# Optimization experiments

Hardware: AMD Instinct MI355X
Metric: run time of the kernel (lower is better)

## Reference

```python
import jax, jax.numpy as jnp
import numpy as np

B, L, HID, H = 4, 1024, 1024, 16
D = HID // H  # 64

def setup_inputs() -> dict:
    key = jax.random.key(0)
    ks = jax.random.split(key, 9)
    s = 0.02
    return {
        'query_states': jax.random.normal(ks[0], (B, L, HID), jnp.float32),
        'key_states':   jax.random.normal(ks[1], (B, L, HID), jnp.float32),
        'value_states': jax.random.normal(ks[2], (B, L, HID), jnp.float32),
        'Wq': jax.random.normal(ks[3], (HID, HID), jnp.float32) * s,
        'bq': jnp.zeros((HID,), jnp.float32),
        'Wk': jax.random.normal(ks[4], (HID, HID), jnp.float32) * s,
        'bk': jnp.zeros((HID,), jnp.float32),
        'Wv': jax.random.normal(ks[5], (HID, HID), jnp.float32) * s,
        'bv': jnp.zeros((HID,), jnp.float32),
        'Wo': jax.random.normal(ks[6], (HID, HID), jnp.float32) * s,
        'bo': jnp.zeros((HID,), jnp.float32),
        'rel_pos_enc': jax.random.normal(ks[7], (2 * L - 1, D), jnp.float32),
    }

def _split_heads(x):
    # [B,L,HID] -> [B,H,L,D]
    return x.reshape(B, L, H, D).transpose(0, 2, 1, 3)

def reference(query_states, key_states, value_states, Wq, bq, Wk, bk, Wv, bv, Wo, bo, rel_pos_enc):
    q = _split_heads(query_states @ Wq + bq)  # [B,H,L,D]
    k = _split_heads(key_states @ Wk + bk)
    v = _split_heads(value_states @ Wv + bv)
    scores = jnp.einsum('bhld,bhrd->bhlr', q, k)
    # relative position bias
    pos = jnp.arange(L)
    distance = pos[:, None] - pos[None, :] + L - 1          # [L,L] in [0, 2L-2]
    pos_emb = rel_pos_enc[distance]                          # [L,L,D]
    scores = scores + jnp.einsum('bhld,lrd->bhlr', q, pos_emb)
    scores = scores / jnp.sqrt(jnp.asarray(D, scores.dtype))
    probs = jax.nn.softmax(scores, axis=-1)                  # dropout p=0 (eval)
    ctx = jnp.einsum('bhlr,bhrd->bhld', probs, v)
    ctx = ctx.transpose(0, 2, 1, 3).reshape(B, L, HID)
    out = ctx @ Wo + bo
    return (out, probs)
```

## Files before the change

### kernel.cpp

```cpp
#include <hip/hip_runtime.h>

typedef __bf16 bf16_t;
typedef bf16_t bf16x8 __attribute__((ext_vector_type(8)));
typedef bf16_t bf16x4 __attribute__((ext_vector_type(4)));
typedef float f32x16 __attribute__((ext_vector_type(16)));
typedef float f32x4v __attribute__((ext_vector_type(4)));
typedef unsigned int u32;

#define DEVI __device__ __forceinline__

DEVI f32x16 zero16() {
  f32x16 z;
#pragma unroll
  for (int i = 0; i < 16; ++i) z[i] = 0.0f;
  return z;
}

DEVI void gload16(const bf16_t* g, const unsigned short* l) {
  __builtin_amdgcn_global_load_lds(
      (const __attribute__((address_space(1))) u32*)g,
      (__attribute__((address_space(3))) u32*)l, 16, 0, 0);
}

union U16B { bf16x8 v; uint4 u; unsigned short s[8]; };
union U4B  { bf16_t h[4]; uint2 u; };

__global__ __launch_bounds__(256) void prep_kernel(
    const float* __restrict__ W0, const float* __restrict__ W1,
    const float* __restrict__ W2, const float* __restrict__ W3,
    bf16_t* __restrict__ T0, bf16_t* __restrict__ T1,
    bf16_t* __restrict__ T2, bf16_t* __restrict__ T3,
    const float* __restrict__ xq, const float* __restrict__ xk,
    const float* __restrict__ xv, const float* __restrict__ relE,
    bf16_t* __restrict__ xqb, bf16_t* __restrict__ xkb,
    bf16_t* __restrict__ xvb, bf16_t* __restrict__ Eb) {
  __shared__ float T[64][65];
  const int bid = blockIdx.x;
  const int tid = threadIdx.x;
  if (bid < 1024) {
    const int sel = bid >> 8;
    const float* W = sel == 0 ? W0 : sel == 1 ? W1 : sel == 2 ? W2 : W3;
    bf16_t* Wt = sel == 0 ? T0 : sel == 1 ? T1 : sel == 2 ? T2 : T3;
    const int bx = bid & 255;
    const int tx = bx & 15, ty = bx >> 4;
    const int k0 = ty * 64, n0 = tx * 64;
    {
      const int r = tid >> 4, c4 = (tid & 15) * 4;
#pragma unroll
      for (int rr = 0; rr < 64; rr += 16) {
        float4 v = *reinterpret_cast<const float4*>(&W[(size_t)(k0 + r + rr) * 1024 + n0 + c4]);
        T[r + rr][c4 + 0] = v.x; T[r + rr][c4 + 1] = v.y;
        T[r + rr][c4 + 2] = v.z; T[r + rr][c4 + 3] = v.w;
      }
    }
    __syncthreads();
    {
      const int r = tid >> 3, c8 = (tid & 7) * 8;
#pragma unroll
      for (int rr = 0; rr < 64; rr += 32) {
        U16B p;
#pragma unroll
        for (int i = 0; i < 8; ++i) p.v[i] = (bf16_t)T[c8 + i][r + rr];
        *reinterpret_cast<uint4*>(&Wt[(size_t)(n0 + r + rr) * 1024 + k0 + c8]) = p.u;
      }
    }
  } else {
    for (int u = (bid - 1024) * 256 + tid; u < 3178496; u += 2048 * 256) {
      if (u < 3145728) {
        const int which = u >> 20;
        const float* src = which == 0 ? xq : which == 1 ? xk : xv;
        bf16_t* dst = which == 0 ? xqb : which == 1 ? xkb : xvb;
        const size_t off = (size_t)(u & 1048575) * 4;
        float4 v = *reinterpret_cast<const float4*>(&src[off]);
        U4B p;
        p.h[0] = (bf16_t)v.x; p.h[1] = (bf16_t)v.y; p.h[2] = (bf16_t)v.z; p.h[3] = (bf16_t)v.w;
        *reinterpret_cast<uint2*>(&dst[off]) = p.u;
      } else {
        const int q = u - 3145728;
        U4B p;
        if (q < 32752) {
          float4 v = *reinterpret_cast<const float4*>(&relE[(size_t)q * 4]);
          p.h[0] = (bf16_t)v.x; p.h[1] = (bf16_t)v.y; p.h[2] = (bf16_t)v.z; p.h[3] = (bf16_t)v.w;
        } else {
          p.h[0] = p.h[1] = p.h[2] = p.h[3] = (bf16_t)0.0f;
        }
        *reinterpret_cast<uint2*>(&Eb[(size_t)q * 4]) = p.u;
      }
    }
  }
}

#define ROWMAP(reg) (((reg) & 3) + 8 * ((reg) >> 2) + 4 * hi)

__global__ __launch_bounds__(512, 2) void gemm_qkv_kernel(
    const bf16_t* __restrict__ A0, const bf16_t* __restrict__ A1,
    const bf16_t* __restrict__ A2, const bf16_t* __restrict__ W0,
    const bf16_t* __restrict__ W1, const bf16_t* __restrict__ W2,
    const float* __restrict__ b0, const float* __restrict__ b1,
    const float* __restrict__ b2, bf16_t* __restrict__ O0,
    bf16_t* __restrict__ O1, bf16_t* __restrict__ O2) {
  __shared__ __align__(16) unsigned short As[2][256][64];
  __shared__ __align__(16) unsigned short Bs[2][256][64];
  const int f = blockIdx.x;
  const int fp = (f & 7) * 24 + (f >> 3);
  const int op = fp >> 6;
  const int r = fp & 63;
  const bf16_t* Ap = op == 0 ? A0 : op == 1 ? A1 : A2;
  const bf16_t* Wt = op == 0 ? W0 : op == 1 ? W1 : W2;
  const float* bias = op == 0 ? b0 : op == 1 ? b1 : b2;
  bf16_t* Out = op == 0 ? O0 : op == 1 ? O1 : O2;
  const int m0 = (r >> 2) * 256, n0 = (r & 3) * 256;
  const int tid = threadIdx.x;
  const int lane = tid & 63, wave = tid >> 6;
  const int hi = lane >> 5, ln = lane & 31;
  const int wr = wave >> 2, wc = wave & 3;
  const int srow = lane >> 3, scol = lane & 7;

  f32x16 acc[4][2];
#pragma unroll
  for (int rt = 0; rt < 4; ++rt) { acc[rt][0] = zero16(); acc[rt][1] = zero16(); }

#define STAGE(kt, buf)                                                              \
  {                                                                                 \
    _Pragma("unroll")                                                               \
    for (int j = 0; j < 4; ++j) {                                                   \
      const int rowbase = wave * 32 + j * 8;                                        \
      const int row = rowbase + srow;                                               \
      const int gc = scol ^ (row & 7);                                              \
      gload16(&Ap[(size_t)(m0 + row) * 1024 + (kt) * 64 + gc * 8],                  \
              &As[buf][rowbase][0]);                                                \
      gload16(&Wt[(size_t)(n0 + row) * 1024 + (kt) * 64 + gc * 8],                  \
              &Bs[buf][rowbase][0]);                                                \
    }                                                                               \
  }

  STAGE(0, 0);
  STAGE(1, 1);

  for (int kt = 0; kt < 16; ++kt) {
    const int cur = kt & 1;
    if (kt < 15) {
      asm volatile("s_waitcnt vmcnt(8)" ::: "memory");
    } else {
      asm volatile("s_waitcnt vmcnt(0)" ::: "memory");
    }
    __builtin_amdgcn_s_barrier();
    __builtin_amdgcn_sched_barrier(0);
#pragma unroll
    for (int kk = 0; kk < 4; ++kk) {
      const int ch = kk * 2 + hi;
      bf16x8 a[4], b[2];
#pragma unroll
      for (int rt = 0; rt < 4; ++rt) {
        const int ar = wr * 128 + rt * 32 + ln;
        a[rt] = *reinterpret_cast<const bf16x8*>(&As[cur][ar][(ch ^ (ar & 7)) * 8]);
      }
#pragma unroll
      for (int ct = 0; ct < 2; ++ct) {
        const int br = wc * 64 + ct * 32 + ln;
        b[ct] = *reinterpret_cast<const bf16x8*>(&Bs[cur][br][(ch ^ (br & 7)) * 8]);
      }
#pragma unroll
      for (int rt = 0; rt < 4; ++rt)
#pragma unroll
        for (int ct = 0; ct < 2; ++ct)
          acc[rt][ct] = __builtin_amdgcn_mfma_f32_32x32x16_bf16(a[rt], b[ct], acc[rt][ct], 0, 0, 0);
    }
    __builtin_amdgcn_sched_barrier(0);
    __builtin_amdgcn_s_barrier();
    __builtin_amdgcn_sched_barrier(0);
    if (kt + 2 < 16) STAGE(kt + 2, cur);
  }
#undef STAGE

#pragma unroll
  for (int ct = 0; ct < 2; ++ct) {
    const int nc = n0 + wc * 64 + ct * 32 + ln;
    const float bv = bias[nc];
    const int h = nc >> 6, d = nc & 63;
    if (op < 2) {
#pragma unroll
      for (int rt = 0; rt < 4; ++rt)
#pragma unroll
        for (int reg = 0; reg < 16; ++reg) {
          const int mr = m0 + wr * 128 + rt * 32 + ROWMAP(reg);
          const int b = mr >> 10, l = mr & 1023;
          Out[(((size_t)(b * 16 + h)) * 1024 + l) * 64 + d] =
              (bf16_t)(acc[rt][ct][reg] + bv);
        }
    } else {
#pragma unroll
      for (int rt = 0; rt < 4; ++rt)
#pragma unroll
        for (int g = 0; g < 4; ++g) {
          const int l4 = m0 + wr * 128 + rt * 32 + g * 8 + 4 * hi;
          const int b = l4 >> 10, ll = l4 & 1023;
          U4B p;
#pragma unroll
          for (int j = 0; j < 4; ++j) p.h[j] = (bf16_t)(acc[rt][ct][g * 4 + j] + bv);
          *reinterpret_cast<uint2*>(
              &Out[(((size_t)(b * 16 + h)) * 64 + d) * 1024 + ll]) = p.u;
        }
    }
  }
}

__global__ __launch_bounds__(256) void gemm_o_kernel(
    const bf16_t* __restrict__ A0, const bf16_t* __restrict__ W0,
    const float* __restrict__ b0, float* __restrict__ O0) {
  __shared__ __align__(16) unsigned short As[2][128][64];
  __shared__ __align__(16) unsigned short Bs[2][128][64];
  const int f = blockIdx.x;
  const int fp = (f & 7) * 32 + (f >> 3);
  const int r = fp;
  const int m0 = (r >> 3) * 128, n0 = (r & 7) * 128;
  const int tid = threadIdx.x;
  const int lane = tid & 63, wave = tid >> 6;
  const int hi = lane >> 5, ln = lane & 31;
  const int wr = wave >> 1, wc = wave & 1;
  const int srow = lane >> 3, scol = lane & 7;

  f32x16 acc[2][2];
  acc[0][0] = zero16(); acc[0][1] = zero16();
  acc[1][0] = zero16(); acc[1][1] = zero16();

#define STAGE_O(kt, buf)                                                            \
  {                                                                                 \
    _Pragma("unroll")                                                               \
    for (int j = 0; j < 4; ++j) {                                                   \
      const int rowbase = wave * 32 + j * 8;                                        \
      const int row = rowbase + srow;                                               \
      const int gc = scol ^ (row & 7);                                              \
      gload16(&A0[(size_t)(m0 + row) * 1024 + (kt) * 64 + gc * 8],                  \
              &As[buf][rowbase][0]);                                                \
      gload16(&W0[(size_t)(n0 + row) * 1024 + (kt) * 64 + gc * 8],                  \
              &Bs[buf][rowbase][0]);                                                \
    }                                                                               \
  }

  STAGE_O(0, 0);
  STAGE_O(1, 1);

  for (int kt = 0; kt < 16; ++kt) {
    const int cur = kt & 1;
    if (kt < 15) {
      asm volatile("s_waitcnt vmcnt(8)" ::: "memory");
    } else {
      asm volatile("s_waitcnt vmcnt(0)" ::: "memory");
    }
    __builtin_amdgcn_s_barrier();
    __builtin_amdgcn_sched_barrier(0);
#pragma unroll
    for (int kk = 0; kk < 4; ++kk) {
      const int ch = kk * 2 + hi;
      const int ar0 = wr * 64 + ln, ar1 = ar0 + 32;
      const int br0 = wc * 64 + ln, br1 = br0 + 32;
      bf16x8 a0 = *reinterpret_cast<const bf16x8*>(&As[cur][ar0][(ch ^ (ar0 & 7)) * 8]);
      bf16x8 a1 = *reinterpret_cast<const bf16x8*>(&As[cur][ar1][(ch ^ (ar1 & 7)) * 8]);
      bf16x8 bb0 = *reinterpret_cast<const bf16x8*>(&Bs[cur][br0][(ch ^ (br0 & 7)) * 8]);
      bf16x8 bb1 = *reinterpret_cast<const bf16x8*>(&Bs[cur][br1][(ch ^ (br1 & 7)) * 8]);
      acc[0][0] = __builtin_amdgcn_mfma_f32_32x32x16_bf16(a0, bb0, acc[0][0], 0, 0, 0);
      acc[0][1] = __builtin_amdgcn_mfma_f32_32x32x16_bf16(a0, bb1, acc[0][1], 0, 0, 0);
      acc[1][0] = __builtin_amdgcn_mfma_f32_32x32x16_bf16(a1, bb0, acc[1][0], 0, 0, 0);
      acc[1][1] = __builtin_amdgcn_mfma_f32_32x32x16_bf16(a1, bb1, acc[1][1], 0, 0, 0);
    }
    __builtin_amdgcn_sched_barrier(0);
    __builtin_amdgcn_s_barrier();
    __builtin_amdgcn_sched_barrier(0);
    if (kt + 2 < 16) STAGE_O(kt + 2, cur);
  }
#undef STAGE_O

#pragma unroll
  for (int cb = 0; cb < 2; ++cb) {
    const int nc = n0 + wc * 64 + cb * 32 + ln;
    const float bv = b0[nc];
#pragma unroll
    for (int rb = 0; rb < 2; ++rb)
#pragma unroll
      for (int reg = 0; reg < 16; ++reg) {
        const int mr = m0 + wr * 64 + rb * 32 + ROWMAP(reg);
        O0[(size_t)mr * 1024 + nc] = acc[rb][cb][reg] + bv;
      }
  }
}

__global__ __launch_bounds__(512, 4) void attn_kernel(
    const bf16_t* __restrict__ q, const bf16_t* __restrict__ k,
    const bf16_t* __restrict__ vt, const bf16_t* __restrict__ E,
    float* __restrict__ probs, bf16_t* __restrict__ ctx) {
  __shared__ __align__(16) unsigned short Pbuf[8][32][128];
  __shared__ float rstat[32][9];
  const int f = blockIdx.x;
  const int fp = (f & 7) * 256 + (f >> 3);
  const int bh = fp >> 5;
  const int l0 = (fp & 31) * 32;
  const int tid = threadIdx.x;
  const int lane = tid & 63, wave = tid >> 6;
  const int hi = lane >> 5, ln = lane & 31;
  const bf16_t* qb = q + (size_t)bh * 1024 * 64;
  const bf16_t* kb = k + (size_t)bh * 1024 * 64;
  const bf16_t* vb = vt + (size_t)bh * 64 * 1024;
  const int rbase = wave * 128;
  const int b0 = l0 - rbase + 992;

  bf16x8 qf[4];
#pragma unroll
  for (int kk = 0; kk < 4; ++kk)
    qf[kk] = *reinterpret_cast<const bf16x8*>(&qb[(size_t)(l0 + ln) * 64 + kk * 16 + hi * 8]);

  f32x16 tpre = zero16();
  __builtin_amdgcn_s_setprio(1);
#pragma unroll
  for (int kk = 0; kk < 4; ++kk) {
    bf16x8 e = *reinterpret_cast<const bf16x8*>(
        &E[(size_t)(b0 + 32 + ln) * 64 + kk * 16 + hi * 8]);
    tpre = __builtin_amdgcn_mfma_f32_32x32x16_bf16(qf[kk], e, tpre, 0, 0, 0);
  }
  __builtin_amdgcn_s_setprio(0);

#pragma unroll
  for (int t = 0; t < 4; ++t) {
    const int r0 = rbase + t * 32;
    f32x16 acc = zero16();
    f32x16 tcur = zero16();
    __builtin_amdgcn_s_setprio(1);
#pragma unroll
    for (int kk = 0; kk < 4; ++kk) {
      bf16x8 kf = *reinterpret_cast<const bf16x8*>(
          &kb[(size_t)(r0 + ln) * 64 + kk * 16 + hi * 8]);
      acc = __builtin_amdgcn_mfma_f32_32x32x16_bf16(qf[kk], kf, acc, 0, 0, 0);
      bf16x8 e = *reinterpret_cast<const bf16x8*>(
          &E[(size_t)(b0 - 32 * t + ln) * 64 + kk * 16 + hi * 8]);
      tcur = __builtin_amdgcn_mfma_f32_32x32x16_bf16(qf[kk], e, tcur, 0, 0, 0);
    }
    __builtin_amdgcn_s_setprio(0);
#pragma unroll
    for (int reg = 0; reg < 16; ++reg) {
      const int i = ROWMAP(reg);
      const int w = i - ln + 31;
      const int src = (w & 31) + (hi << 5);
      acc[reg] += __shfl((ln >= i) ? tcur[reg] : tpre[reg], src, 64);
    }
    const int col = t * 32 + ln;
#pragma unroll
    for (int reg = 0; reg < 16; ++reg) {
      const int i = ROWMAP(reg);
      union { bf16_t h; unsigned short u; } cv;
      cv.h = (bf16_t)exp2f(acc[reg] * 0.1803368801f);
      Pbuf[wave][i][((col >> 3) ^ (i & 7)) * 8 + (col & 7)] = cv.u;
    }
    tpre = tcur;
  }

  {
    float s = 0.0f;
#pragma unroll
    for (int g = 0; g < 8; ++g) {
      const int cg = hi * 8 + g;
      bf16x8 pv = *reinterpret_cast<const bf16x8*>(
          &Pbuf[wave][ln][((cg ^ (ln & 7))) * 8]);
#pragma unroll
      for (int e = 0; e < 8; ++e) s += (float)pv[e];
    }
    s += __shfl_xor(s, 32, 64);
    if (hi == 0) rstat[ln][wave] = s;
  }

  f32x16 pv0 = zero16(), pv1 = zero16();
  __builtin_amdgcn_s_setprio(1);
#pragma unroll
  for (int kk = 0; kk < 8; ++kk) {
    const int ch = kk * 2 + hi;
    bf16x8 pa = *reinterpret_cast<const bf16x8*>(&Pbuf[wave][ln][(ch ^ (ln & 7)) * 8]);
    bf16x8 v0 = *reinterpret_cast<const bf16x8*>(
        &vb[(size_t)ln * 1024 + rbase + kk * 16 + hi * 8]);
    bf16x8 v1 = *reinterpret_cast<const bf16x8*>(
        &vb[(size_t)(32 + ln) * 1024 + rbase + kk * 16 + hi * 8]);
    pv0 = __builtin_amdgcn_mfma_f32_32x32x16_bf16(pa, v0, pv0, 0, 0, 0);
    pv1 = __builtin_amdgcn_mfma_f32_32x32x16_bf16(pa, v1, pv1, 0, 0, 0);
  }
  __builtin_amdgcn_s_setprio(0);

  __syncthreads();

  float inv;
  {
    float s = 0.0f;
#pragma unroll
    for (int w = 0; w < 8; ++w) s += rstat[ln][w];
    inv = 1.0f / s;
  }

  float* pb = probs + ((size_t)bh * 1024 + l0) * 1024;
#pragma unroll
  for (int it = 0; it < 16; ++it) {
    const int r = it * 2 + hi;
    const float invr = __shfl(inv, r, 64);
    const int g = ln >> 1;
    bf16x4 pv = *reinterpret_cast<const bf16x4*>(
        &Pbuf[wave][r][(g ^ (r & 7)) * 8 + (ln & 1) * 4]);
    f32x4v o;
    o[0] = (float)pv[0] * invr; o[1] = (float)pv[1] * invr;
    o[2] = (float)pv[2] * invr; o[3] = (float)pv[3] * invr;
    __builtin_nontemporal_store(
        o, reinterpret_cast<f32x4v*>(&pb[(size_t)r * 1024 + rbase + ln * 4]));
  }

  float* cred = reinterpret_cast<float*>(&Pbuf[0][0][0]);
  if (wave < 4) {
#pragma unroll
    for (int reg = 0; reg < 16; ++reg) {
      const int i = ROWMAP(reg);
      cred[((size_t)wave * 32 + i) * 64 + ln] = pv0[reg];
      cred[((size_t)wave * 32 + i) * 64 + 32 + ln] = pv1[reg];
    }
  }
  __syncthreads();
  if (wave >= 4) {
    const int s = wave - 4;
#pragma unroll
    for (int reg = 0; reg < 16; ++reg) {
      const int i = ROWMAP(reg);
      cred[((size_t)s * 32 + i) * 64 + ln] += pv0[reg];
      cred[((size_t)s * 32 + i) * 64 + 32 + ln] += pv1[reg];
    }
  }
  __syncthreads();
  {
    const int i = tid >> 4, d0 = (tid & 15) * 4;
    float4 a = *reinterpret_cast<const float4*>(&cred[(size_t)(0 * 32 + i) * 64 + d0]);
#pragma unroll
    for (int s = 1; s < 4; ++s) {
      float4 b = *reinterpret_cast<const float4*>(&cred[(size_t)(s * 32 + i) * 64 + d0]);
      a.x += b.x; a.y += b.y; a.z += b.z; a.w += b.w;
    }
    const float invr = __shfl(inv, i, 64);
    U4B o;
    o.h[0] = (bf16_t)(a.x * invr); o.h[1] = (bf16_t)(a.y * invr);
    o.h[2] = (bf16_t)(a.z * invr); o.h[3] = (bf16_t)(a.w * invr);
    const int b = bh >> 4, h = bh & 15;
    *reinterpret_cast<uint2*>(&ctx[((((size_t)b * 1024) + l0 + i) * 16 + h) * 64 + d0]) = o.u;
  }
}

extern "C" void kernel_launch(void* const* d_in, const int* in_sizes, int n_in,
                              void* d_out, int out_size, void* d_ws, size_t ws_size,
                              hipStream_t stream) {
  const float* xq = (const float*)d_in[0];
  const float* xk = (const float*)d_in[1];
  const float* xv = (const float*)d_in[2];
  const float* Wq = (const float*)d_in[3];
  const float* bq = (const float*)d_in[4];
  const float* Wk = (const float*)d_in[5];
  const float* bk = (const float*)d_in[6];
  const float* Wv = (const float*)d_in[7];
  const float* bv = (const float*)d_in[8];
  const float* Wo = (const float*)d_in[9];
  const float* bo = (const float*)d_in[10];
  const float* relE = (const float*)d_in[11];

  char* ws = (char*)d_ws;
  const size_t MB2 = 1u << 21;
  bf16_t* WtQ = (bf16_t*)(ws + 0 * MB2);
  bf16_t* WtK = (bf16_t*)(ws + 1 * MB2);
  bf16_t* WtV = (bf16_t*)(ws + 2 * MB2);
  bf16_t* WtO = (bf16_t*)(ws + 3 * MB2);
  bf16_t* Eb  = (bf16_t*)(ws + 4 * MB2);
  bf16_t* qb  = (bf16_t*)(ws + 4 * MB2 + (1u << 19));
  bf16_t* kb  = qb + (size_t)4 * 16 * 1024 * 64;
  bf16_t* vtb = kb + (size_t)4 * 16 * 1024 * 64;
  bf16_t* ctxb = vtb + (size_t)4 * 16 * 1024 * 64;

  float* outp = (float*)d_out;
  float* probs = outp + (size_t)4 * 1024 * 1024;
  bf16_t* xqb = (bf16_t*)probs;
  bf16_t* xkb = xqb + (size_t)4 * 1024 * 1024;
  bf16_t* xvb = xkb + (size_t)4 * 1024 * 1024;

  prep_kernel<<<3072, 256, 0, stream>>>(Wq, Wk, Wv, Wo, WtQ, WtK, WtV, WtO,
                                        xq, xk, xv, relE, xqb, xkb, xvb, Eb);
  gemm_qkv_kernel<<<192, 512, 0, stream>>>(xqb, xkb, xvb, WtQ, WtK, WtV,
                                           bq, bk, bv, qb, kb, vtb);
  attn_kernel<<<2048, 512, 0, stream>>>(qb, kb, vtb, Eb, probs, ctxb);
  gemm_o_kernel<<<256, 256, 0, stream>>>(ctxb, WtO, bo, outp);
}
```

Baseline: 196.7 us.

## Fuse fp32-to-bf16 activation conversion into QKV GEMM A-tile loading

Drops the separate pass in the prep kernel that turned the fp32 query/key/value inputs into bf16 scratch buffers. The QKV GEMM now reads the fp32 activations into registers, converts them, and writes swizzled bf16 into LDS. Those register loads run one k-step ahead alongside the existing async weight loads. This removes a full write and re-read of about 24 MB of bf16 intermediates, but A-tile loads no longer go directly to LDS. The GEMM also reads twice as many bytes per A element, adds register pressure, and needs extra waitcnt and barrier handling.

```diff
diff --git a/kernel.cpp b/kernel.cpp
--- a/kernel.cpp
+++ b/kernel.cpp
@@ -30,10 +30,7 @@
     const float* __restrict__ W2, const float* __restrict__ W3,
     bf16_t* __restrict__ T0, bf16_t* __restrict__ T1,
     bf16_t* __restrict__ T2, bf16_t* __restrict__ T3,
-    const float* __restrict__ xq, const float* __restrict__ xk,
-    const float* __restrict__ xv, const float* __restrict__ relE,
-    bf16_t* __restrict__ xqb, bf16_t* __restrict__ xkb,
-    bf16_t* __restrict__ xvb, bf16_t* __restrict__ Eb) {
+    const float* __restrict__ relE, bf16_t* __restrict__ Eb) {
   __shared__ float T[64][65];
   const int bid = blockIdx.x;
   const int tid = threadIdx.x;
@@ -65,36 +62,23 @@
       }
     }
   } else {
-    for (int u = (bid - 1024) * 256 + tid; u < 3178496; u += 2048 * 256) {
-      if (u < 3145728) {
-        const int which = u >> 20;
-        const float* src = which == 0 ? xq : which == 1 ? xk : xv;
-        bf16_t* dst = which == 0 ? xqb : which == 1 ? xkb : xvb;
-        const size_t off = (size_t)(u & 1048575) * 4;
-        float4 v = *reinterpret_cast<const float4*>(&src[off]);
-        U4B p;
-        p.h[0] = (bf16_t)v.x; p.h[1] = (bf16_t)v.y; p.h[2] = (bf16_t)v.z; p.h[3] = (bf16_t)v.w;
-        *reinterpret_cast<uint2*>(&dst[off]) = p.u;
-      } else {
-        const int q = u - 3145728;
-        U4B p;
-        if (q < 32752) {
-          float4 v = *reinterpret_cast<const float4*>(&relE[(size_t)q * 4]);
-          p.h[0] = (bf16_t)v.x; p.h[1] = (bf16_t)v.y; p.h[2] = (bf16_t)v.z; p.h[3] = (bf16_t)v.w;
-        } else {
-          p.h[0] = p.h[1] = p.h[2] = p.h[3] = (bf16_t)0.0f;
-        }
-        *reinterpret_cast<uint2*>(&Eb[(size_t)q * 4]) = p.u;
-      }
-    }
+    const int q = (bid - 1024) * 256 + tid;
+    U4B p;
+    if (q < 32752) {
+      float4 v = *reinterpret_cast<const float4*>(&relE[(size_t)q * 4]);
+      p.h[0] = (bf16_t)v.x; p.h[1] = (bf16_t)v.y; p.h[2] = (bf16_t)v.z; p.h[3] = (bf16_t)v.w;
+    } else {
+      p.h[0] = p.h[1] = p.h[2] = p.h[3] = (bf16_t)0.0f;
+    }
+    *reinterpret_cast<uint2*>(&Eb[(size_t)q * 4]) = p.u;
   }
 }
 
 #define ROWMAP(reg) (((reg) & 3) + 8 * ((reg) >> 2) + 4 * hi)
 
 __global__ __launch_bounds__(512, 2) void gemm_qkv_kernel(
-    const bf16_t* __restrict__ A0, const bf16_t* __restrict__ A1,
-    const bf16_t* __restrict__ A2, const bf16_t* __restrict__ W0,
+    const float* __restrict__ X0, const float* __restrict__ X1,
+    const float* __restrict__ X2, const bf16_t* __restrict__ W0,
     const bf16_t* __restrict__ W1, const bf16_t* __restrict__ W2,
     const float* __restrict__ b0, const float* __restrict__ b1,
     const float* __restrict__ b2, bf16_t* __restrict__ O0,
@@ -105,7 +89,7 @@
   const int fp = (f & 7) * 24 + (f >> 3);
   const int op = fp >> 6;
   const int r = fp & 63;
-  const bf16_t* Ap = op == 0 ? A0 : op == 1 ? A1 : A2;
+  const float* Xp = op == 0 ? X0 : op == 1 ? X1 : X2;
   const bf16_t* Wt = op == 0 ? W0 : op == 1 ? W1 : W2;
   const float* bias = op == 0 ? b0 : op == 1 ? b1 : b2;
   bf16_t* Out = op == 0 ? O0 : op == 1 ? O1 : O2;
@@ -120,30 +104,61 @@
 #pragma unroll
   for (int rt = 0; rt < 4; ++rt) { acc[rt][0] = zero16(); acc[rt][1] = zero16(); }
 
-#define STAGE(kt, buf)                                                              \
+  float4 fA[4][2];
+
+#define ALOADR(kt)                                                                  \
+  {                                                                                 \
+    _Pragma("unroll")                                                               \
+    for (int j = 0; j < 4; ++j) {                                                   \
+      const int row = wave * 32 + j * 8 + srow;                                     \
+      const float* src = &Xp[(size_t)(m0 + row) * 1024 + (kt) * 64 + scol * 8];     \
+      fA[j][0] = *reinterpret_cast<const float4*>(src);                             \
+      fA[j][1] = *reinterpret_cast<const float4*>(src + 4);                         \
+    }                                                                               \
+  }
+
+#define ACVW(buf)                                                                   \
+  {                                                                                 \
+    _Pragma("unroll")                                                               \
+    for (int j = 0; j < 4; ++j) {                                                   \
+      const int row = wave * 32 + j * 8 + srow;                                     \
+      U16B p;                                                                       \
+      p.v[0] = (bf16_t)fA[j][0].x; p.v[1] = (bf16_t)fA[j][0].y;                     \
+      p.v[2] = (bf16_t)fA[j][0].z; p.v[3] = (bf16_t)fA[j][0].w;                     \
+      p.v[4] = (bf16_t)fA[j][1].x; p.v[5] = (bf16_t)fA[j][1].y;                     \
+      p.v[6] = (bf16_t)fA[j][1].z; p.v[7] = (bf16_t)fA[j][1].w;                     \
+      *reinterpret_cast<uint4*>(&As[buf][row][(scol ^ (row & 7)) * 8]) = p.u;       \
+    }                                                                               \
+  }
+
+#define BGL(kt, buf)                                                                \
   {                                                                                 \
     _Pragma("unroll")                                                               \
     for (int j = 0; j < 4; ++j) {                                                   \
       const int rowbase = wave * 32 + j * 8;                                        \
       const int row = rowbase + srow;                                               \
       const int gc = scol ^ (row & 7);                                              \
-      gload16(&Ap[(size_t)(m0 + row) * 1024 + (kt) * 64 + gc * 8],                  \
-              &As[buf][rowbase][0]);                                                \
       gload16(&Wt[(size_t)(n0 + row) * 1024 + (kt) * 64 + gc * 8],                  \
               &Bs[buf][rowbase][0]);                                                \
     }                                                                               \
   }
 
-  STAGE(0, 0);
-  STAGE(1, 1);
+  ALOADR(0);
+  asm volatile("s_waitcnt vmcnt(0)" ::: "memory");
+  __builtin_amdgcn_sched_barrier(0);
+  ACVW(0);
+  BGL(0, 0);
+  ALOADR(1);
+  BGL(1, 1);
 
   for (int kt = 0; kt < 16; ++kt) {
     const int cur = kt & 1;
     if (kt < 15) {
-      asm volatile("s_waitcnt vmcnt(8)" ::: "memory");
+      asm volatile("s_waitcnt vmcnt(12)" ::: "memory");
     } else {
       asm volatile("s_waitcnt vmcnt(0)" ::: "memory");
     }
+    asm volatile("s_waitcnt lgkmcnt(0)" ::: "memory");
     __builtin_amdgcn_s_barrier();
     __builtin_amdgcn_sched_barrier(0);
 #pragma unroll
@@ -167,11 +182,20 @@
           acc[rt][ct] = __builtin_amdgcn_mfma_f32_32x32x16_bf16(a[rt], b[ct], acc[rt][ct], 0, 0, 0);
     }
     __builtin_amdgcn_sched_barrier(0);
+    if (kt + 1 < 16) {
+      asm volatile("s_waitcnt vmcnt(4)" ::: "memory");
+      __builtin_amdgcn_sched_barrier(0);
+      ACVW(cur ^ 1);
+      if (kt + 2 < 16) ALOADR(kt + 2);
+    }
+    asm volatile("s_waitcnt lgkmcnt(0)" ::: "memory");
     __builtin_amdgcn_s_barrier();
     __builtin_amdgcn_sched_barrier(0);
-    if (kt + 2 < 16) STAGE(kt + 2, cur);
-  }
-#undef STAGE
+    if (kt + 2 < 16) BGL(kt + 2, cur);
+  }
+#undef ALOADR
+#undef ACVW
+#undef BGL
 
 #pragma unroll
   for (int ct = 0; ct < 2; ++ct) {
@@ -474,13 +498,10 @@
 
   float* outp = (float*)d_out;
   float* probs = outp + (size_t)4 * 1024 * 1024;
-  bf16_t* xqb = (bf16_t*)probs;
-  bf16_t* xkb = xqb + (size_t)4 * 1024 * 1024;
-  bf16_t* xvb = xkb + (size_t)4 * 1024 * 1024;
-
-  prep_kernel<<<3072, 256, 0, stream>>>(Wq, Wk, Wv, Wo, WtQ, WtK, WtV, WtO,
-                                        xq, xk, xv, relE, xqb, xkb, xvb, Eb);
-  gemm_qkv_kernel<<<192, 512, 0, stream>>>(xqb, xkb, xvb, WtQ, WtK, WtV,
+
+  prep_kernel<<<1152, 256, 0, stream>>>(Wq, Wk, Wv, Wo, WtQ, WtK, WtV, WtO,
+                                        relE, Eb);
+  gemm_qkv_kernel<<<192, 512, 0, stream>>>(xq, xk, xv, WtQ, WtK, WtV,
                                            bq, bk, bv, qb, kb, vtb);
   attn_kernel<<<2048, 512, 0, stream>>>(qb, kb, vtb, Eb, probs, ctxb);
   gemm_o_kernel<<<256, 256, 0, stream>>>(ctxb, WtO, bo, outp);
```

Result: faster. 190.8 us (median of 3 runs) (-3.0%).
